# Performance work log

Measured on AMD Instinct MI355X. Metric: run time of the kernel, lower is better.

Reference implementation:

```python
import jax, jax.numpy as jnp
import numpy as np

N_USER, N_ITEM, D, K, E = 80000, 40000, 128, 10, 2000000

def _mlp(x, w1, b1, w2, b2, w3, b3):
    # MLP from source: linear->tanh->linear->tanh->linear->L2 normalize (eval mode, dropout off)
    x = jnp.tanh(x @ w1 + b1)
    x = jnp.tanh(x @ w2 + b2)
    x = x @ w3 + b3
    return x / jnp.maximum(jnp.linalg.norm(x, axis=-1, keepdims=True), 1e-12)

def setup_inputs() -> dict:
    key = jax.random.key(0)
    ks = jax.random.split(key, 24)
    s = 0.05
    inp = {
        'uemb_s': jax.random.normal(ks[0], (N_USER, D), jnp.float32),
        'iemb_s': jax.random.normal(ks[1], (N_ITEM, D), jnp.float32),
        'uemb_t': jax.random.normal(ks[2], (N_USER, D), jnp.float32),
        'u_emb_sp': jax.random.normal(ks[3], (N_USER, D), jnp.float32),
        'edge_user': jax.random.randint(ks[4], (E,), 0, N_USER, jnp.int32),
        'edge_item': jax.random.randint(ks[5], (E,), 0, N_ITEM, jnp.int32),
        # meta nets
        'Wu': jax.random.normal(ks[6], (4 * D, D), jnp.float32) * s,
        'bu': jnp.zeros((D,), jnp.float32),
        'Wi': jax.random.normal(ks[7], (2 * D, D), jnp.float32) * s,
        'bi': jnp.zeros((D,), jnp.float32),
        # mlp1: D -> D*K -> D//2 -> D*K
        'm1w1': jax.random.normal(ks[8], (D, D * K), jnp.float32) * s,
        'm1b1': jnp.zeros((D * K,), jnp.float32),
        'm1w2': jax.random.normal(ks[9], (D * K, D // 2), jnp.float32) * s,
        'm1b2': jnp.zeros((D // 2,), jnp.float32),
        'm1w3': jax.random.normal(ks[10], (D // 2, D * K), jnp.float32) * s,
        'm1b3': jnp.zeros((D * K,), jnp.float32),
        # mlp2: D -> D*K -> D//2 -> D*K
        'm2w1': jax.random.normal(ks[11], (D, D * K), jnp.float32) * s,
        'm2b1': jnp.zeros((D * K,), jnp.float32),
        'm2w2': jax.random.normal(ks[12], (D * K, D // 2), jnp.float32) * s,
        'm2b2': jnp.zeros((D // 2,), jnp.float32),
        'm2w3': jax.random.normal(ks[13], (D // 2, D * K), jnp.float32) * s,
        'm2b3': jnp.zeros((D * K,), jnp.float32),
    }
    return inp

def reference(uemb_s, iemb_s, uemb_t, u_emb_sp, edge_user, edge_item,
              Wu, bu, Wi, bi,
              m1w1, m1b1, m1w2, m1b2, m1w3, m1b3,
              m2w1, m2b1, m2w2, m2b2, m2w3, m2b3):
    # spmm with all-ones values == gather + segment_sum over the bipartite edge list
    neighbors_u = jax.ops.segment_sum(iemb_s[edge_item], edge_user, num_segments=N_USER)  # [U, D]
    tmp_embu = jax.lax.stop_gradient(
        jnp.concatenate([uemb_s, uemb_t, u_emb_sp, neighbors_u], axis=1)) @ Wu + bu       # [U, D]
    neighbors_i = jax.ops.segment_sum(((uemb_s + u_emb_sp) * 0.5)[edge_user], edge_item,
                                      num_segments=N_ITEM)                               # [I, D]
    tmp_embi = jax.lax.stop_gradient(
        jnp.concatenate([iemb_s, neighbors_i], axis=1)) @ Wi + bi                         # [I, D]
    metau = _mlp(tmp_embu, m1w1, m1b1, m1w2, m1b2, m1w3, m1b3).reshape(-1, D, K)          # [U, D, K]
    metai = _mlp(tmp_embi, m2w1, m2b1, m2w2, m2b2, m2w3, m2b3).reshape(-1, K, D)          # [I, K, D]
    meta_biasu = jnp.mean(metau, axis=0)  # [D, K]
    meta_biasi = jnp.mean(metai, axis=0)  # [K, D]
    low_weightu = jax.nn.softmax(metau + meta_biasu, axis=1)
    low_weighti = jax.nn.softmax(metai + meta_biasi, axis=1)
    return (low_weightu, low_weighti)
```

## Files before the change

### kernel.cpp

```cpp
#include <hip/hip_runtime.h>
#include <hip/hip_bf16.h>

#define D_ 128
#define DK_ 1280
#define K_ 10

typedef __attribute__((ext_vector_type(8))) short bh8;
typedef __attribute__((ext_vector_type(4))) short bh4;
typedef __attribute__((ext_vector_type(4))) float f32x4;

__device__ __forceinline__ short f2b(float f) {
    unsigned u = __builtin_bit_cast(unsigned, f);
    u += 0x7fffu + ((u >> 16) & 1u);
    return (short)(u >> 16);
}
__device__ __forceinline__ float b2f(short s) {
    unsigned u = ((unsigned)(unsigned short)s) << 16;
    return __builtin_bit_cast(float, u);
}
__device__ __forceinline__ float tanh_fast(float x) {
    float e = __expf(2.f * x);
    return 1.f - __fdividef(2.f, e + 1.f);
}
__device__ __forceinline__ f32x4 mfma16(bh8 a, bh8 b, f32x4 c) {
    return __builtin_amdgcn_mfma_f32_16x16x32_bf16(a, b, c, 0, 0, 0);
}

__device__ __forceinline__ int blk_excl_scan(int v, int t) {
    __shared__ int wp[4];
    int lane = t & 63, w = t >> 6;
    int s = v;
    for (int o = 1; o < 64; o <<= 1) {
        int pv = __shfl_up(s, o);
        if (lane >= o) s += pv;
    }
    if (lane == 63) wp[w] = s;
    __syncthreads();
    if (t == 0) {
        int a = 0;
#pragma unroll
        for (int k = 0; k < 4; ++k) { int x = wp[k]; wp[k] = a; a += x; }
    }
    __syncthreads();
    int r = s - v + wp[w];
    __syncthreads();
    return r;
}

__global__ __launch_bounds__(256) void cvt_all(
    const float* __restrict__ us, const float* __restrict__ ut,
    const float* __restrict__ usp, const float* __restrict__ is_,
    short* __restrict__ usb, short* __restrict__ utb,
    short* __restrict__ uspb, short* __restrict__ uavg, short* __restrict__ isb,
    int n4u, int n4i)
{
    int i = blockIdx.x * 256 + threadIdx.x;
    if (i < n4u) {
        float4 a = ((const float4*)us)[i];
        float4 b = ((const float4*)ut)[i];
        float4 c = ((const float4*)usp)[i];
        bh4 sa, sb, sc, sv;
        sa[0] = f2b(a.x); sa[1] = f2b(a.y); sa[2] = f2b(a.z); sa[3] = f2b(a.w);
        sb[0] = f2b(b.x); sb[1] = f2b(b.y); sb[2] = f2b(b.z); sb[3] = f2b(b.w);
        sc[0] = f2b(c.x); sc[1] = f2b(c.y); sc[2] = f2b(c.z); sc[3] = f2b(c.w);
        sv[0] = f2b(0.5f * (a.x + c.x)); sv[1] = f2b(0.5f * (a.y + c.y));
        sv[2] = f2b(0.5f * (a.z + c.z)); sv[3] = f2b(0.5f * (a.w + c.w));
        ((bh4*)usb)[i] = sa; ((bh4*)utb)[i] = sb;
        ((bh4*)uspb)[i] = sc; ((bh4*)uavg)[i] = sv;
    } else if (i < n4u + n4i) {
        int j = i - n4u;
        float4 v = ((const float4*)is_)[j];
        bh4 s;
        s[0] = f2b(v.x); s[1] = f2b(v.y); s[2] = f2b(v.z); s[3] = f2b(v.w);
        ((bh4*)isb)[j] = s;
    }
}

struct PackArgs {
    const float* W[8];
    short* o[8];
    int K[8];
    int N[8];
};
__global__ __launch_bounds__(256) void pack_all(PackArgs pa)
{
    int seg = blockIdx.y;
    int K = pa.K[seg], N = pa.N[seg];
    int total = K * N;
    int o = blockIdx.x * 256 + threadIdx.x;
    if (o >= total) return;
    const float* W = pa.W[seg];
    short* out = pa.o[seg];
    int j    = o & 7;
    int lane = (o >> 3) & 63;
    int rest = o >> 9;
    int KK = K >> 5;
    int kk = rest % KK;
    int tile = rest / KK;
    int k = kk * 32 + (lane >> 4) * 8 + j;
    int n = tile * 16 + (lane & 15);
    out[o] = f2b(W[(size_t)k * N + n]);
}

__global__ __launch_bounds__(256) void bhist_kernel(
    const int* __restrict__ eu, const int* __restrict__ ei,
    int* __restrict__ bcu, int* __restrict__ bci,
    int E, int shu, int shi, int nbu, int nbi)
{
    __shared__ int hu[160], hi[160];
    int t = threadIdx.x;
    int base = blockIdx.x * 4096;
    if (t < 160) { hu[t] = 0; hi[t] = 0; }
    __syncthreads();
    int n = min(4096, E - base);
#pragma unroll 4
    for (int k = 0; k < 16; ++k) {
        int idx = k * 256 + t;
        if (idx < n) {
            atomicAdd(&hu[eu[base + idx] >> shu], 1);
            atomicAdd(&hi[ei[base + idx] >> shi], 1);
        }
    }
    __syncthreads();
    if (t < nbu && hu[t]) atomicAdd(&bcu[t], hu[t]);
    if (t < nbi && hi[t]) atomicAdd(&bci[t], hi[t]);
}

__global__ __launch_bounds__(256) void binit_kernel(
    const int* __restrict__ bcu, int* __restrict__ gcu, int* __restrict__ bbu, int nbu,
    const int* __restrict__ bci, int* __restrict__ gci, int* __restrict__ bbi, int nbi,
    int E)
{
    int t = threadIdx.x;
    {
        int v = (t < nbu) ? bcu[t] : 0;
        int ex = blk_excl_scan(v, t);
        if (t < nbu) { gcu[t] = ex; bbu[t] = ex; }
        if (t == 0) bbu[nbu] = E;
    }
    __syncthreads();
    {
        int v = (t < nbi) ? bci[t] : 0;
        int ex = blk_excl_scan(v, t);
        if (t < nbi) { gci[t] = ex; bbi[t] = ex; }
        if (t == 0) bbi[nbi] = E;
    }
}

__global__ __launch_bounds__(256) void partition_kernel(
    const int* __restrict__ eu, const int* __restrict__ ei,
    int* __restrict__ gcu, int* __restrict__ gci,
    uint2* __restrict__ ebu, uint2* __restrict__ ebi,
    int E, int shu, int shi, int nbu, int nbi)
{
    __shared__ int hu[160], hi[160];
    int t = threadIdx.x;
    int base = blockIdx.x * 4096;
    if (t < 160) { hu[t] = 0; hi[t] = 0; }
    __syncthreads();
    int n = min(4096, E - base);
    int us[16], is_[16];
#pragma unroll 4
    for (int k = 0; k < 16; ++k) {
        int idx = k * 256 + t;
        if (idx < n) {
            us[k] = eu[base + idx];
            is_[k] = ei[base + idx];
            atomicAdd(&hu[us[k] >> shu], 1);
            atomicAdd(&hi[is_[k] >> shi], 1);
        } else us[k] = -1;
    }
    __syncthreads();
    if (t < nbu) { int c = hu[t]; hu[t] = c ? atomicAdd(&gcu[t], c) : 0; }
    if (t < nbi) { int c = hi[t]; hi[t] = c ? atomicAdd(&gci[t], c) : 0; }
    __syncthreads();
#pragma unroll 4
    for (int k = 0; k < 16; ++k) {
        if (us[k] >= 0) {
            int p1 = atomicAdd(&hu[us[k] >> shu], 1);
            ebu[p1] = make_uint2((unsigned)us[k], (unsigned)is_[k]);
            int p2 = atomicAdd(&hi[is_[k] >> shi], 1);
            ebi[p2] = make_uint2((unsigned)is_[k], (unsigned)us[k]);
        }
    }
}

__global__ __launch_bounds__(256) void fill2_all(
    const uint2* __restrict__ ebu, const int* __restrict__ bbu,
    int* __restrict__ off_u, int* __restrict__ end_u, int* __restrict__ adj_u,
    int NBU, int U,
    const uint2* __restrict__ ebi, const int* __restrict__ bbi,
    int* __restrict__ off_i, int* __restrict__ end_i, int* __restrict__ adj_i, int I)
{
    __shared__ int lcnt[512];
    __shared__ int lcur[512];
    bool isU = (int)blockIdx.x < NBU;
    const uint2* ebuf = isU ? ebu : ebi;
    const int* bbase  = isU ? bbu : bbi;
    int* off  = isU ? off_u : off_i;
    int* end_ = isU ? end_u : end_i;
    int* adj  = isU ? adj_u : adj_i;
    int span_sh = isU ? 9 : 8;
    int nrows = isU ? U : I;
    int b = isU ? blockIdx.x : blockIdx.x - NBU;

    int t = threadIdx.x;
    int rbase = b << span_sh;
    int span = min(1 << span_sh, nrows - rbase);
    int regbeg = bbase[b], regend = bbase[b + 1];
    for (int j = t; j < span; j += 256) lcnt[j] = 0;
    __syncthreads();
    for (int e = regbeg + t; e < regend; e += 256)
        atomicAdd(&lcnt[ebuf[e].x - rbase], 1);
    __syncthreads();
    int c0 = (2 * t < span) ? lcnt[2 * t] : 0;
    int c1 = (2 * t + 1 < span) ? lcnt[2 * t + 1] : 0;
    int ex = blk_excl_scan(c0 + c1, t);
    if (2 * t < span) {
        int beg = regbeg + ex;
        off[rbase + 2 * t] = beg;
        end_[rbase + 2 * t] = beg + c0;
        lcur[2 * t] = beg;
    }
    if (2 * t + 1 < span) {
        int beg = regbeg + ex + c0;
        off[rbase + 2 * t + 1] = beg;
        end_[rbase + 2 * t + 1] = beg + c1;
        lcur[2 * t + 1] = beg;
    }
    __syncthreads();
    for (int e = regbeg + t; e < regend; e += 256) {
        uint2 p = ebuf[e];
        int slot = atomicAdd(&lcur[p.x - rbase], 1);
        adj[slot] = (int)p.y;
    }
}

__global__ __launch_bounds__(256) void gather_all(
    const short* __restrict__ embU, const short* __restrict__ embI,
    const int* __restrict__ off_u, const int* __restrict__ end_u, const int* __restrict__ adj_u,
    const int* __restrict__ off_i, const int* __restrict__ end_i, const int* __restrict__ adj_i,
    short* __restrict__ nub, short* __restrict__ nib, int U, int I)
{
    int gw = (blockIdx.x * 256 + threadIdx.x) >> 6;
    int lane = threadIdx.x & 63;
    const short* emb; const int *offp, *endp, *adjp; short* outp; int row;
    if (gw < U)          { emb = embU; offp = off_u; endp = end_u; adjp = adj_u; outp = nub; row = gw; }
    else if (gw < U + I) { emb = embI; offp = off_i; endp = end_i; adjp = adj_i; outp = nib; row = gw - U; }
    else return;

    int beg = offp[row], end = endp[row];
    float ax = 0.f, ay = 0.f;
    int j = beg;
    for (; j + 3 < end; j += 4) {
        unsigned a = *(const unsigned*)(emb + (size_t)adjp[j]     * D_ + lane * 2);
        unsigned b = *(const unsigned*)(emb + (size_t)adjp[j + 1] * D_ + lane * 2);
        unsigned c = *(const unsigned*)(emb + (size_t)adjp[j + 2] * D_ + lane * 2);
        unsigned d = *(const unsigned*)(emb + (size_t)adjp[j + 3] * D_ + lane * 2);
        ax += b2f((short)(a & 0xffff)) + b2f((short)(b & 0xffff))
            + b2f((short)(c & 0xffff)) + b2f((short)(d & 0xffff));
        ay += b2f((short)(a >> 16)) + b2f((short)(b >> 16))
            + b2f((short)(c >> 16)) + b2f((short)(d >> 16));
    }
    for (; j < end; ++j) {
        unsigned a = *(const unsigned*)(emb + (size_t)adjp[j] * D_ + lane * 2);
        ax += b2f((short)(a & 0xffff));
        ay += b2f((short)(a >> 16));
    }
    unsigned o = ((unsigned)(unsigned short)f2b(ay) << 16) | (unsigned short)(unsigned)f2b(ax);
    *(unsigned*)(outp + (size_t)row * D_ + lane * 2) = o;
}

struct MlpArgs {
    const short *uA0, *uA1, *uA2, *uA3;
    const short *iA0, *iA1;
    const short *uWg, *uW1, *uW2, *uW3;
    const short *iWg, *iW1, *iW2, *iW3;
    const float *ubg, *ub1, *ub2, *ub3;
    const float *ibg, *ib1, *ib2, *ib3;
    short *uY, *iY;
    float *uNrm, *iNrm;
    int UB;
};

__global__ __launch_bounds__(256, 4) void fused_mlp_all(MlpArgs P)
{
    __shared__ char pool[35328];
    short* x2   = (short*)pool;
    short* h1q  = (short*)(pool + 8704);
    short* h2   = (short*)(pool + 29696);
    float* wred = (float*)(pool + 34304);

    const int t = threadIdx.x;
    const int l = t & 63;
    const int w = t >> 6;
    const int lr = l & 15;
    const int lg = l >> 4;

    const bool isU = (int)blockIdx.x < P.UB;
    const int bid = isU ? (int)blockIdx.x : (int)blockIdx.x - P.UB;
    const size_t rb0 = (size_t)bid * 32;
    const int KKG  = isU ? 16 : 8;
    const short* Wg = isU ? P.uWg : P.iWg;
    const short* W1 = isU ? P.uW1 : P.iW1;
    const short* W2 = isU ? P.uW2 : P.iW2;
    const short* W3 = isU ? P.uW3 : P.iW3;
    const float* bg = isU ? P.ubg : P.ibg;
    const float* b1 = isU ? P.ub1 : P.ib1;
    const float* b2 = isU ? P.ub2 : P.ib2;
    const float* b3 = isU ? P.ub3 : P.ib3;
    short* Ybf = isU ? P.uY : P.iY;
    float* Nrm = isU ? P.uNrm : P.iNrm;
    const short* srcs[4];
    if (isU) { srcs[0] = P.uA0; srcs[1] = P.uA1; srcs[2] = P.uA2; srcs[3] = P.uA3; }
    else     { srcs[0] = P.iA0; srcs[1] = P.iA1; srcs[2] = P.iA0; srcs[3] = P.iA1; }

    {
        f32x4 acc[2][2] = {{{0,0,0,0},{0,0,0,0}},{{0,0,0,0},{0,0,0,0}}};
        const short* wp = Wg + (size_t)(2 * w) * KKG * 512 + l * 8;
        const short* wq = wp + (size_t)KKG * 512;
        for (int kk = 0; kk < KKG; ++kk) {
            const short* src = srcs[kk >> 2];
            int coff = (kk & 3) * 32 + lg * 8;
            bh8 x0 = *(const bh8*)(src + (rb0 + lr) * D_ + coff);
            bh8 x1 = *(const bh8*)(src + (rb0 + 16 + lr) * D_ + coff);
            bh8 w0 = *(const bh8*)wp; wp += 512;
            bh8 w1 = *(const bh8*)wq; wq += 512;
            acc[0][0] = mfma16(w0, x0, acc[0][0]);
            acc[1][0] = mfma16(w0, x1, acc[1][0]);
            acc[0][1] = mfma16(w1, x0, acc[0][1]);
            acc[1][1] = mfma16(w1, x1, acc[1][1]);
        }
        float4 c0 = *(const float4*)(bg + (2 * w) * 16 + lg * 4);
        float4 c1 = *(const float4*)(bg + (2 * w + 1) * 16 + lg * 4);
#pragma unroll
        for (int rg = 0; rg < 2; ++rg) {
            bh4 p0, p1;
            p0[0] = f2b(acc[rg][0][0] + c0.x); p0[1] = f2b(acc[rg][0][1] + c0.y);
            p0[2] = f2b(acc[rg][0][2] + c0.z); p0[3] = f2b(acc[rg][0][3] + c0.w);
            p1[0] = f2b(acc[rg][1][0] + c1.x); p1[1] = f2b(acc[rg][1][1] + c1.y);
            p1[2] = f2b(acc[rg][1][2] + c1.z); p1[3] = f2b(acc[rg][1][3] + c1.w);
            *(bh4*)(x2 + (rg * 16 + lr) * 136 + (2 * w) * 16 + lg * 4) = p0;
            *(bh4*)(x2 + (rg * 16 + lr) * 136 + (2 * w + 1) * 16 + lg * 4) = p1;
        }
    }
    __syncthreads();

    bh8 xf[2][4];
#pragma unroll
    for (int rg = 0; rg < 2; ++rg)
#pragma unroll
        for (int kk = 0; kk < 4; ++kk)
            xf[rg][kk] = *(const bh8*)(x2 + (rg * 16 + lr) * 136 + kk * 32 + lg * 8);

    f32x4 c2[2][2] = {{{0,0,0,0},{0,0,0,0}},{{0,0,0,0},{0,0,0,0}}};
#pragma unroll 1
    for (int q = 0; q < 4; ++q) {
        const short* wp = W1 + (size_t)(q * 20 + w * 5) * 2048 + l * 8;
        const float* bp = b1 + (q * 20 + w * 5) * 16 + lg * 4;
#pragma unroll 1
        for (int tt = 0; tt < 5; ++tt) {
            f32x4 a0 = {0,0,0,0}, a1 = a0;
#pragma unroll
            for (int kk = 0; kk < 4; ++kk) {
                bh8 wf = *(const bh8*)wp; wp += 512;
                a0 = mfma16(wf, xf[0][kk], a0);
                a1 = mfma16(wf, xf[1][kk], a1);
            }
            float4 bv = *(const float4*)bp; bp += 16;
            bh4 pk0, pk1;
            pk0[0] = f2b(tanh_fast(a0[0] + bv.x)); pk0[1] = f2b(tanh_fast(a0[1] + bv.y));
            pk0[2] = f2b(tanh_fast(a0[2] + bv.z)); pk0[3] = f2b(tanh_fast(a0[3] + bv.w));
            pk1[0] = f2b(tanh_fast(a1[0] + bv.x)); pk1[1] = f2b(tanh_fast(a1[1] + bv.y));
            pk1[2] = f2b(tanh_fast(a1[2] + bv.z)); pk1[3] = f2b(tanh_fast(a1[3] + bv.w));
            int lt = w * 5 + tt;
            *(bh4*)(h1q + lr * 328 + lt * 16 + lg * 4) = pk0;
            *(bh4*)(h1q + (16 + lr) * 328 + lt * 16 + lg * 4) = pk1;
        }
        __syncthreads();
        const short* wp2 = W2 + (size_t)(w * 40 + q * 10) * 512 + l * 8;
        const short* hq0 = h1q + lr * 328 + lg * 8;
        const short* hq1 = h1q + (16 + lr) * 328 + lg * 8;
#pragma unroll 2
        for (int kk = 0; kk < 10; ++kk) {
            bh8 wf = *(const bh8*)wp2; wp2 += 512;
            bh8 h0 = *(const bh8*)(hq0 + kk * 32);
            bh8 h1v = *(const bh8*)(hq1 + kk * 32);
            if (kk & 1) { c2[0][1] = mfma16(wf, h0, c2[0][1]); c2[1][1] = mfma16(wf, h1v, c2[1][1]); }
            else        { c2[0][0] = mfma16(wf, h0, c2[0][0]); c2[1][0] = mfma16(wf, h1v, c2[1][0]); }
        }
        __syncthreads();
    }

    {
        float4 bv = *(const float4*)(b2 + w * 16 + lg * 4);
#pragma unroll
        for (int rg = 0; rg < 2; ++rg) {
            bh4 p2;
            p2[0] = f2b(tanh_fast(c2[rg][0][0] + c2[rg][1][0] + bv.x));
            p2[1] = f2b(tanh_fast(c2[rg][0][1] + c2[rg][1][1] + bv.y));
            p2[2] = f2b(tanh_fast(c2[rg][0][2] + c2[rg][1][2] + bv.z));
            p2[3] = f2b(tanh_fast(c2[rg][0][3] + c2[rg][1][3] + bv.w));
            *(bh4*)(h2 + (rg * 16 + lr) * 72 + w * 16 + lg * 4) = p2;
        }
    }
    __syncthreads();

    {
        bh8 hf[2][2];
#pragma unroll
        for (int rg = 0; rg < 2; ++rg) {
            hf[rg][0] = *(const bh8*)(h2 + (rg * 16 + lr) * 72 + lg * 8);
            hf[rg][1] = *(const bh8*)(h2 + (rg * 16 + lr) * 72 + 32 + lg * 8);
        }
        float ssq0 = 0.f, ssq1 = 0.f;
        const short* wp3 = W3 + (size_t)(w * 20) * 1024 + l * 8;
        const float* bp3 = b3 + w * 320 + lg * 4;
        short* dst0 = Ybf + (rb0 + lr) * DK_ + w * 320 + lg * 4;
        short* dst1 = Ybf + (rb0 + 16 + lr) * DK_ + w * 320 + lg * 4;
#pragma unroll 2
        for (int tt = 0; tt < 20; ++tt) {
            bh8 w0 = *(const bh8*)(wp3 + tt * 1024);
            bh8 w1 = *(const bh8*)(wp3 + tt * 1024 + 512);
            float4 bv = *(const float4*)(bp3 + tt * 16);
            f32x4 a0 = {0,0,0,0}, a1 = a0;
            a0 = mfma16(w0, hf[0][0], a0); a0 = mfma16(w1, hf[0][1], a0);
            a1 = mfma16(w0, hf[1][0], a1); a1 = mfma16(w1, hf[1][1], a1);
            float v00 = a0[0] + bv.x, v01 = a0[1] + bv.y, v02 = a0[2] + bv.z, v03 = a0[3] + bv.w;
            float v10 = a1[0] + bv.x, v11 = a1[1] + bv.y, v12 = a1[2] + bv.z, v13 = a1[3] + bv.w;
            ssq0 = fmaf(v00, v00, ssq0); ssq0 = fmaf(v01, v01, ssq0);
            ssq0 = fmaf(v02, v02, ssq0); ssq0 = fmaf(v03, v03, ssq0);
            ssq1 = fmaf(v10, v10, ssq1); ssq1 = fmaf(v11, v11, ssq1);
            ssq1 = fmaf(v12, v12, ssq1); ssq1 = fmaf(v13, v13, ssq1);
            bh4 o0, o1;
            o0[0] = f2b(v00); o0[1] = f2b(v01); o0[2] = f2b(v02); o0[3] = f2b(v03);
            o1[0] = f2b(v10); o1[1] = f2b(v11); o1[2] = f2b(v12); o1[3] = f2b(v13);
            *(bh4*)(dst0 + tt * 16) = o0;
            *(bh4*)(dst1 + tt * 16) = o1;
        }
        ssq0 += __shfl_xor(ssq0, 16); ssq0 += __shfl_xor(ssq0, 32);
        ssq1 += __shfl_xor(ssq1, 16); ssq1 += __shfl_xor(ssq1, 32);
        if (l < 16) {
            wred[w * 32 + l] = ssq0;
            wred[w * 32 + 16 + l] = ssq1;
        }
    }
    __syncthreads();
    if (t < 32) {
        float s = wred[t] + wred[32 + t] + wred[64 + t] + wred[96 + t];
        Nrm[rb0 + t] = 1.f / fmaxf(sqrtf(s), 1e-12f);
    }
}

__global__ __launch_bounds__(256) void finalize_bias(
    const short* __restrict__ Yu, const short* __restrict__ Yi,
    const float* __restrict__ nrmU, const float* __restrict__ nrmI,
    float* __restrict__ bsu, float* __restrict__ bsi, int U, int I, int NCH)
{
    int z = blockIdx.y;
    const short* Y = z ? Yi : Yu;
    const float* nr = z ? nrmI : nrmU;
    float* dst = z ? bsi : bsu;
    int M = z ? I : U;
    int chunk = (M + NCH - 1) / NCH;
    int r0 = blockIdx.x * chunk;
    int r1 = min(M, r0 + chunk);
    if (r0 >= r1) return;
    int t = threadIdx.x;
    float s0 = 0.f, s1 = 0.f, s2 = 0.f, s3 = 0.f, s4 = 0.f;
    for (int r = r0; r < r1; ++r) {
        const short* row = Y + (size_t)r * DK_;
        float nv = nr[r];
        s0 += b2f(row[t]) * nv;
        s1 += b2f(row[256 + t]) * nv;
        s2 += b2f(row[512 + t]) * nv;
        s3 += b2f(row[768 + t]) * nv;
        s4 += b2f(row[1024 + t]) * nv;
    }
    atomicAdd(&dst[t], s0);
    atomicAdd(&dst[256 + t], s1);
    atomicAdd(&dst[512 + t], s2);
    atomicAdd(&dst[768 + t], s3);
    atomicAdd(&dst[1024 + t], s4);
}

__global__ __launch_bounds__(64) void softmax_all(
    const short* __restrict__ Yu, const short* __restrict__ Yi,
    const float* __restrict__ nrmU, const float* __restrict__ nrmI,
    const float* __restrict__ bsu, const float* __restrict__ bsi,
    float invU, float invI,
    float* __restrict__ outu, float* __restrict__ outi, int U, int I)
{
    __shared__ float rowb[DK_];
    int b = blockIdx.x;
    int t = threadIdx.x;
    if (b < U) {
        size_t base = (size_t)b * DK_;
        float nrm = nrmU[b];
        for (int i = t; i < DK_ / 4; i += 64) {
            uint2 a = ((const uint2*)(Yu + base))[i];
            float4 bv = ((const float4*)bsu)[i];
            rowb[4 * i + 0] = b2f((short)(a.x & 0xffff)) * nrm + bv.x * invU;
            rowb[4 * i + 1] = b2f((short)(a.x >> 16))    * nrm + bv.y * invU;
            rowb[4 * i + 2] = b2f((short)(a.y & 0xffff)) * nrm + bv.z * invU;
            rowb[4 * i + 3] = b2f((short)(a.y >> 16))    * nrm + bv.w * invU;
        }
        __syncthreads();
#pragma unroll 1
        for (int k = 0; k < K_; ++k) {
            float v0 = rowb[t * K_ + k];
            float v1 = rowb[(t + 64) * K_ + k];
            float m = fmaxf(v0, v1);
            for (int off = 32; off; off >>= 1) m = fmaxf(m, __shfl_xor(m, off));
            float e0 = expf(v0 - m), e1 = expf(v1 - m);
            float s = e0 + e1;
            for (int off = 32; off; off >>= 1) s += __shfl_xor(s, off);
            float rs = 1.f / s;
            rowb[t * K_ + k] = e0 * rs;
            rowb[(t + 64) * K_ + k] = e1 * rs;
        }
        __syncthreads();
        for (int i = t; i < DK_ / 4; i += 64)
            ((float4*)(outu + base))[i] = ((const float4*)rowb)[i];
    } else {
        int it = b - U;
        if (it >= I) return;
        size_t base = (size_t)it * DK_;
        float nrm = nrmI[it];
        float v0[K_], v1[K_];
        float m0 = -1e30f, m1 = -1e30f;
#pragma unroll
        for (int k = 0; k < K_; ++k) {
            unsigned a = *(const unsigned*)(Yi + base + k * D_ + 2 * t);
            float2 bv = ((const float2*)(bsi + k * D_))[t];
            v0[k] = b2f((short)(a & 0xffff)) * nrm + bv.x * invI;
            v1[k] = b2f((short)(a >> 16))    * nrm + bv.y * invI;
            m0 = fmaxf(m0, v0[k]); m1 = fmaxf(m1, v1[k]);
        }
        float s0 = 0.f, s1 = 0.f;
#pragma unroll
        for (int k = 0; k < K_; ++k) {
            v0[k] = expf(v0[k] - m0); s0 += v0[k];
            v1[k] = expf(v1[k] - m1); s1 += v1[k];
        }
        float r0 = 1.f / s0, r1 = 1.f / s1;
#pragma unroll
        for (int k = 0; k < K_; ++k) {
            float2 o; o.x = v0[k] * r0; o.y = v1[k] * r1;
            ((float2*)(outi + base + k * D_))[t] = o;
        }
    }
}

extern "C" void kernel_launch(void* const* d_in, const int* in_sizes, int n_in,
                              void* d_out, int out_size, void* d_ws, size_t ws_size,
                              hipStream_t stream)
{
    const float* uemb_s   = (const float*)d_in[0];
    const float* iemb_s   = (const float*)d_in[1];
    const float* uemb_t   = (const float*)d_in[2];
    const float* u_emb_sp = (const float*)d_in[3];
    const int*   eu       = (const int*)d_in[4];
    const int*   ei       = (const int*)d_in[5];
    const float* Wu  = (const float*)d_in[6];
    const float* bu  = (const float*)d_in[7];
    const float* Wi  = (const float*)d_in[8];
    const float* bi  = (const float*)d_in[9];
    const float* m1w1 = (const float*)d_in[10];
    const float* m1b1 = (const float*)d_in[11];
    const float* m1w2 = (const float*)d_in[12];
    const float* m1b2 = (const float*)d_in[13];
    const float* m1w3 = (const float*)d_in[14];
    const float* m1b3 = (const float*)d_in[15];
    const float* m2w1 = (const float*)d_in[16];
    const float* m2b1 = (const float*)d_in[17];
    const float* m2w2 = (const float*)d_in[18];
    const float* m2b2 = (const float*)d_in[19];
    const float* m2w3 = (const float*)d_in[20];
    const float* m2b3 = (const float*)d_in[21];

    const int U = in_sizes[0] / D_;
    const int I = in_sizes[1] / D_;
    const int E = in_sizes[4];

    const int SHU = 9, SHI = 8;
    const int NBU = (U + 511) >> 9;
    const int NBI = (I + 255) >> 8;
    const int UB = U / 32, IB = I / 32;

    char* p = (char*)d_ws;
    auto alloc = [&](size_t bytes) { char* r = p; p += (bytes + 255) & ~(size_t)255; return r; };

    short* usb  = (short*)alloc((size_t)U * D_ * 2);
    short* utb  = (short*)alloc((size_t)U * D_ * 2);
    short* uspb = (short*)alloc((size_t)U * D_ * 2);
    short* uavg = (short*)alloc((size_t)U * D_ * 2);
    short* isb  = (short*)alloc((size_t)I * D_ * 2);
    short* nub  = (short*)alloc((size_t)U * D_ * 2);
    short* nib  = (short*)alloc((size_t)I * D_ * 2);
    short* ybu  = (short*)alloc((size_t)U * DK_ * 2);
    short* ybi  = (short*)alloc((size_t)I * DK_ * 2);
    float* nrmU = (float*)alloc((size_t)U * 4);
    float* nrmI = (float*)alloc((size_t)I * 4);
    short* WgU  = (short*)alloc(512 * 128 * 2);
    short* WgI  = (short*)alloc(256 * 128 * 2);
    short* W1U  = (short*)alloc(128 * 1280 * 2);
    short* W2U  = (short*)alloc(1280 * 64 * 2);
    short* W3U  = (short*)alloc(64 * 1280 * 2);
    short* W1I  = (short*)alloc(128 * 1280 * 2);
    short* W2I  = (short*)alloc(1280 * 64 * 2);
    short* W3I  = (short*)alloc(64 * 1280 * 2);
    int*   zbuf = (int*)alloc((320 + 2 * DK_) * 4);
    int* bcnt_u = zbuf;
    int* bcnt_i = zbuf + 160;
    float* bsu  = (float*)(zbuf + 320);
    float* bsi  = bsu + DK_;
    int* gcur_u = (int*)alloc(160 * 4);
    int* gcur_i = (int*)alloc(160 * 4);
    int* bbase_u = (int*)alloc(161 * 4);
    int* bbase_i = (int*)alloc(161 * 4);
    int* off_u  = (int*)alloc((size_t)U * 4);
    int* end_u  = (int*)alloc((size_t)U * 4);
    int* off_i  = (int*)alloc((size_t)I * 4);
    int* end_i  = (int*)alloc((size_t)I * 4);
    uint2* ebu  = (uint2*)alloc((size_t)E * 8);
    uint2* ebi  = (uint2*)alloc((size_t)E * 8);
    int* adj_u  = (int*)alloc((size_t)E * 4);
    int* adj_i  = (int*)alloc((size_t)E * 4);

    float* outu = (float*)d_out;
    float* outi = outu + (size_t)U * DK_;

    hipMemsetAsync(zbuf, 0, (320 + 2 * DK_) * 4, stream);

    int n4u = U * D_ / 4, n4i = I * D_ / 4;
    cvt_all<<<(n4u + n4i + 255) / 256, 256, 0, stream>>>(
        uemb_s, uemb_t, u_emb_sp, iemb_s, usb, utb, uspb, uavg, isb, n4u, n4i);

    PackArgs pa;
    pa.W[0] = Wu;   pa.o[0] = WgU; pa.K[0] = 512;  pa.N[0] = 128;
    pa.W[1] = Wi;   pa.o[1] = WgI; pa.K[1] = 256;  pa.N[1] = 128;
    pa.W[2] = m1w1; pa.o[2] = W1U; pa.K[2] = 128;  pa.N[2] = 1280;
    pa.W[3] = m1w2; pa.o[3] = W2U; pa.K[3] = 1280; pa.N[3] = 64;
    pa.W[4] = m1w3; pa.o[4] = W3U; pa.K[4] = 64;   pa.N[4] = 1280;
    pa.W[5] = m2w1; pa.o[5] = W1I; pa.K[5] = 128;  pa.N[5] = 1280;
    pa.W[6] = m2w2; pa.o[6] = W2I; pa.K[6] = 1280; pa.N[6] = 64;
    pa.W[7] = m2w3; pa.o[7] = W3I; pa.K[7] = 64;   pa.N[7] = 1280;
    pack_all<<<dim3(640, 8), 256, 0, stream>>>(pa);

    int pb = (E + 4095) / 4096;
    bhist_kernel<<<pb, 256, 0, stream>>>(eu, ei, bcnt_u, bcnt_i, E, SHU, SHI, NBU, NBI);
    binit_kernel<<<1, 256, 0, stream>>>(bcnt_u, gcur_u, bbase_u, NBU,
                                        bcnt_i, gcur_i, bbase_i, NBI, E);
    partition_kernel<<<pb, 256, 0, stream>>>(eu, ei, gcur_u, gcur_i, ebu, ebi,
                                             E, SHU, SHI, NBU, NBI);
    fill2_all<<<NBU + NBI, 256, 0, stream>>>(ebu, bbase_u, off_u, end_u, adj_u, NBU, U,
                                             ebi, bbase_i, off_i, end_i, adj_i, I);

    gather_all<<<(U + I + 3) / 4, 256, 0, stream>>>(
        isb, uavg, off_u, end_u, adj_u, off_i, end_i, adj_i, nub, nib, U, I);

    MlpArgs ma;
    ma.uA0 = usb; ma.uA1 = utb; ma.uA2 = uspb; ma.uA3 = nub;
    ma.iA0 = isb; ma.iA1 = nib;
    ma.uWg = WgU; ma.uW1 = W1U; ma.uW2 = W2U; ma.uW3 = W3U;
    ma.iWg = WgI; ma.iW1 = W1I; ma.iW2 = W2I; ma.iW3 = W3I;
    ma.ubg = bu; ma.ub1 = m1b1; ma.ub2 = m1b2; ma.ub3 = m1b3;
    ma.ibg = bi; ma.ib1 = m2b1; ma.ib2 = m2b2; ma.ib3 = m2b3;
    ma.uY = ybu; ma.iY = ybi;
    ma.uNrm = nrmU; ma.iNrm = nrmI;
    ma.UB = UB;
    fused_mlp_all<<<UB + IB, 256, 0, stream>>>(ma);

    finalize_bias<<<dim3(256, 2), 256, 0, stream>>>(ybu, ybi, nrmU, nrmI, bsu, bsi, U, I, 256);

    softmax_all<<<U + I, 64, 0, stream>>>(ybu, ybi, nrmU, nrmI, bsu, bsi,
                                          1.0f / (float)U, 1.0f / (float)I, outu, outi, U, I);
}
```

Baseline: 929.4 us.

## Use 64-row MLP tiles, fuse column-mean partials, and pack edge buffers into 32 bits

The fused MLP now processes 64 rows per block instead of 32, so each weight fragment load feeds four row groups of MFMAs. The h1 chunking is restructured to 10 slices of 128 columns, reusing LDS space. The block also computes per-column normalized partial sums for the mean bias and writes them out, so finalize_bias only reduces a small partial buffer instead of re-reading the whole Y matrix. Separately, the partition buffers pack the local row offset and neighbor index into one 32-bit word, halving the edge-bucket traffic. Risks are higher register pressure with fewer blocks launched, and an extra re-read of freshly written Y from cache inside the MLP kernel.

```diff
diff --git a/kernel.cpp b/kernel.cpp
--- a/kernel.cpp
+++ b/kernel.cpp
@@ -150,7 +150,7 @@
 __global__ __launch_bounds__(256) void partition_kernel(
     const int* __restrict__ eu, const int* __restrict__ ei,
     int* __restrict__ gcu, int* __restrict__ gci,
-    uint2* __restrict__ ebu, uint2* __restrict__ ebi,
+    unsigned* __restrict__ ebu, unsigned* __restrict__ ebi,
     int E, int shu, int shi, int nbu, int nbi)
 {
     __shared__ int hu[160], hi[160];
@@ -178,29 +178,31 @@
     for (int k = 0; k < 16; ++k) {
         if (us[k] >= 0) {
             int p1 = atomicAdd(&hu[us[k] >> shu], 1);
-            ebu[p1] = make_uint2((unsigned)us[k], (unsigned)is_[k]);
+            ebu[p1] = ((unsigned)(us[k] & 511) << 16) | (unsigned)is_[k];
             int p2 = atomicAdd(&hi[is_[k] >> shi], 1);
-            ebi[p2] = make_uint2((unsigned)is_[k], (unsigned)us[k]);
+            ebi[p2] = ((unsigned)(is_[k] & 255) << 17) | (unsigned)us[k];
         }
     }
 }
 
 __global__ __launch_bounds__(256) void fill2_all(
-    const uint2* __restrict__ ebu, const int* __restrict__ bbu,
+    const unsigned* __restrict__ ebu, const int* __restrict__ bbu,
     int* __restrict__ off_u, int* __restrict__ end_u, int* __restrict__ adj_u,
     int NBU, int U,
-    const uint2* __restrict__ ebi, const int* __restrict__ bbi,
+    const unsigned* __restrict__ ebi, const int* __restrict__ bbi,
     int* __restrict__ off_i, int* __restrict__ end_i, int* __restrict__ adj_i, int I)
 {
     __shared__ int lcnt[512];
     __shared__ int lcur[512];
     bool isU = (int)blockIdx.x < NBU;
-    const uint2* ebuf = isU ? ebu : ebi;
+    const unsigned* ebuf = isU ? ebu : ebi;
     const int* bbase  = isU ? bbu : bbi;
     int* off  = isU ? off_u : off_i;
     int* end_ = isU ? end_u : end_i;
     int* adj  = isU ? adj_u : adj_i;
     int span_sh = isU ? 9 : 8;
+    int pay_sh = isU ? 16 : 17;
+    unsigned pmask = (1u << pay_sh) - 1u;
     int nrows = isU ? U : I;
     int b = isU ? blockIdx.x : blockIdx.x - NBU;
 
@@ -211,7 +213,7 @@
     for (int j = t; j < span; j += 256) lcnt[j] = 0;
     __syncthreads();
     for (int e = regbeg + t; e < regend; e += 256)
-        atomicAdd(&lcnt[ebuf[e].x - rbase], 1);
+        atomicAdd(&lcnt[ebuf[e] >> pay_sh], 1);
     __syncthreads();
     int c0 = (2 * t < span) ? lcnt[2 * t] : 0;
     int c1 = (2 * t + 1 < span) ? lcnt[2 * t + 1] : 0;
@@ -230,9 +232,9 @@
     }
     __syncthreads();
     for (int e = regbeg + t; e < regend; e += 256) {
-        uint2 p = ebuf[e];
-        int slot = atomicAdd(&lcur[p.x - rbase], 1);
-        adj[slot] = (int)p.y;
+        unsigned p = ebuf[e];
+        int slot = atomicAdd(&lcur[p >> pay_sh], 1);
+        adj[slot] = (int)(p & pmask);
     }
 }
 
@@ -280,16 +282,19 @@
     const float *ibg, *ib1, *ib2, *ib3;
     short *uY, *iY;
     float *uNrm, *iNrm;
+    float *partial;
     int UB;
 };
 
 __global__ __launch_bounds__(256, 4) void fused_mlp_all(MlpArgs P)
 {
-    __shared__ char pool[35328];
+    __shared__ char pool[33024];
     short* x2   = (short*)pool;
-    short* h1q  = (short*)(pool + 8704);
-    short* h2   = (short*)(pool + 29696);
-    float* wred = (float*)(pool + 34304);
+    short* h1q  = (short*)pool;
+    short* h2   = (short*)(pool + 17408);
+    float* wred = (float*)(pool + 26624);
+    float* nrmS = (float*)(pool + 27648);
+    float* part = (float*)(pool + 27904);
 
     const int t = threadIdx.x;
     const int l = t & 63;
@@ -299,7 +304,7 @@
 
     const bool isU = (int)blockIdx.x < P.UB;
     const int bid = isU ? (int)blockIdx.x : (int)blockIdx.x - P.UB;
-    const size_t rb0 = (size_t)bid * 32;
+    const size_t rb0 = (size_t)bid * 64;
     const int KKG  = isU ? 16 : 8;
     const short* Wg = isU ? P.uWg : P.iWg;
     const short* W1 = isU ? P.uW1 : P.iW1;
@@ -316,25 +321,26 @@
     else     { srcs[0] = P.iA0; srcs[1] = P.iA1; srcs[2] = P.iA0; srcs[3] = P.iA1; }
 
     {
-        f32x4 acc[2][2] = {{{0,0,0,0},{0,0,0,0}},{{0,0,0,0},{0,0,0,0}}};
+        f32x4 acc[4][2] = {{{0,0,0,0},{0,0,0,0}},{{0,0,0,0},{0,0,0,0}},
+                           {{0,0,0,0},{0,0,0,0}},{{0,0,0,0},{0,0,0,0}}};
         const short* wp = Wg + (size_t)(2 * w) * KKG * 512 + l * 8;
         const short* wq = wp + (size_t)KKG * 512;
         for (int kk = 0; kk < KKG; ++kk) {
             const short* src = srcs[kk >> 2];
             int coff = (kk & 3) * 32 + lg * 8;
-            bh8 x0 = *(const bh8*)(src + (rb0 + lr) * D_ + coff);
-            bh8 x1 = *(const bh8*)(src + (rb0 + 16 + lr) * D_ + coff);
             bh8 w0 = *(const bh8*)wp; wp += 512;
             bh8 w1 = *(const bh8*)wq; wq += 512;
-            acc[0][0] = mfma16(w0, x0, acc[0][0]);
-            acc[1][0] = mfma16(w0, x1, acc[1][0]);
-            acc[0][1] = mfma16(w1, x0, acc[0][1]);
-            acc[1][1] = mfma16(w1, x1, acc[1][1]);
+#pragma unroll
+            for (int rg = 0; rg < 4; ++rg) {
+                bh8 xv = *(const bh8*)(src + (rb0 + rg * 16 + lr) * D_ + coff);
+                acc[rg][0] = mfma16(w0, xv, acc[rg][0]);
+                acc[rg][1] = mfma16(w1, xv, acc[rg][1]);
+            }
         }
         float4 c0 = *(const float4*)(bg + (2 * w) * 16 + lg * 4);
         float4 c1 = *(const float4*)(bg + (2 * w + 1) * 16 + lg * 4);
 #pragma unroll
-        for (int rg = 0; rg < 2; ++rg) {
+        for (int rg = 0; rg < 4; ++rg) {
             bh4 p0, p1;
             p0[0] = f2b(acc[rg][0][0] + c0.x); p0[1] = f2b(acc[rg][0][1] + c0.y);
             p0[2] = f2b(acc[rg][0][2] + c0.z); p0[3] = f2b(acc[rg][0][3] + c0.w);
@@ -346,48 +352,51 @@
     }
     __syncthreads();
 
-    bh8 xf[2][4];
-#pragma unroll
-    for (int rg = 0; rg < 2; ++rg)
+    bh8 xf[4][4];
+#pragma unroll
+    for (int rg = 0; rg < 4; ++rg)
 #pragma unroll
         for (int kk = 0; kk < 4; ++kk)
             xf[rg][kk] = *(const bh8*)(x2 + (rg * 16 + lr) * 136 + kk * 32 + lg * 8);
-
-    f32x4 c2[2][2] = {{{0,0,0,0},{0,0,0,0}},{{0,0,0,0},{0,0,0,0}}};
+    __syncthreads();
+
+    f32x4 c2[4] = {{0,0,0,0},{0,0,0,0},{0,0,0,0},{0,0,0,0}};
 #pragma unroll 1
-    for (int q = 0; q < 4; ++q) {
-        const short* wp = W1 + (size_t)(q * 20 + w * 5) * 2048 + l * 8;
-        const float* bp = b1 + (q * 20 + w * 5) * 16 + lg * 4;
+    for (int q = 0; q < 10; ++q) {
 #pragma unroll 1
-        for (int tt = 0; tt < 5; ++tt) {
-            f32x4 a0 = {0,0,0,0}, a1 = a0;
+        for (int tt = 0; tt < 2; ++tt) {
+            int gt = q * 8 + w * 2 + tt;
+            const short* wp = W1 + (size_t)gt * 2048 + l * 8;
+            f32x4 a[4] = {{0,0,0,0},{0,0,0,0},{0,0,0,0},{0,0,0,0}};
 #pragma unroll
             for (int kk = 0; kk < 4; ++kk) {
                 bh8 wf = *(const bh8*)wp; wp += 512;
-                a0 = mfma16(wf, xf[0][kk], a0);
-                a1 = mfma16(wf, xf[1][kk], a1);
+#pragma unroll
+                for (int rg = 0; rg < 4; ++rg)
+                    a[rg] = mfma16(wf, xf[rg][kk], a[rg]);
             }
-            float4 bv = *(const float4*)bp; bp += 16;
-            bh4 pk0, pk1;
-            pk0[0] = f2b(tanh_fast(a0[0] + bv.x)); pk0[1] = f2b(tanh_fast(a0[1] + bv.y));
-            pk0[2] = f2b(tanh_fast(a0[2] + bv.z)); pk0[3] = f2b(tanh_fast(a0[3] + bv.w));
-            pk1[0] = f2b(tanh_fast(a1[0] + bv.x)); pk1[1] = f2b(tanh_fast(a1[1] + bv.y));
-            pk1[2] = f2b(tanh_fast(a1[2] + bv.z)); pk1[3] = f2b(tanh_fast(a1[3] + bv.w));
-            int lt = w * 5 + tt;
-            *(bh4*)(h1q + lr * 328 + lt * 16 + lg * 4) = pk0;
-            *(bh4*)(h1q + (16 + lr) * 328 + lt * 16 + lg * 4) = pk1;
+            float4 bv = *(const float4*)(b1 + gt * 16 + lg * 4);
+            int lt = (w * 2 + tt) * 16;
+#pragma unroll
+            for (int rg = 0; rg < 4; ++rg) {
+                bh4 pk;
+                pk[0] = f2b(tanh_fast(a[rg][0] + bv.x));
+                pk[1] = f2b(tanh_fast(a[rg][1] + bv.y));
+                pk[2] = f2b(tanh_fast(a[rg][2] + bv.z));
+                pk[3] = f2b(tanh_fast(a[rg][3] + bv.w));
+                *(bh4*)(h1q + (rg * 16 + lr) * 136 + lt + lg * 4) = pk;
+            }
         }
         __syncthreads();
-        const short* wp2 = W2 + (size_t)(w * 40 + q * 10) * 512 + l * 8;
-        const short* hq0 = h1q + lr * 328 + lg * 8;
-        const short* hq1 = h1q + (16 + lr) * 328 + lg * 8;
-#pragma unroll 2
-        for (int kk = 0; kk < 10; ++kk) {
+        const short* wp2 = W2 + ((size_t)w * 40 + q * 4) * 512 + l * 8;
+#pragma unroll
+        for (int kk = 0; kk < 4; ++kk) {
             bh8 wf = *(const bh8*)wp2; wp2 += 512;
-            bh8 h0 = *(const bh8*)(hq0 + kk * 32);
-            bh8 h1v = *(const bh8*)(hq1 + kk * 32);
-            if (kk & 1) { c2[0][1] = mfma16(wf, h0, c2[0][1]); c2[1][1] = mfma16(wf, h1v, c2[1][1]); }
-            else        { c2[0][0] = mfma16(wf, h0, c2[0][0]); c2[1][0] = mfma16(wf, h1v, c2[1][0]); }
+#pragma unroll
+            for (int rg = 0; rg < 4; ++rg) {
+                bh8 hf = *(const bh8*)(h1q + (rg * 16 + lr) * 136 + kk * 32 + lg * 8);
+                c2[rg] = mfma16(wf, hf, c2[rg]);
+            }
         }
         __syncthreads();
     }
@@ -395,93 +404,111 @@
     {
         float4 bv = *(const float4*)(b2 + w * 16 + lg * 4);
 #pragma unroll
-        for (int rg = 0; rg < 2; ++rg) {
+        for (int rg = 0; rg < 4; ++rg) {
             bh4 p2;
-            p2[0] = f2b(tanh_fast(c2[rg][0][0] + c2[rg][1][0] + bv.x));
-            p2[1] = f2b(tanh_fast(c2[rg][0][1] + c2[rg][1][1] + bv.y));
-            p2[2] = f2b(tanh_fast(c2[rg][0][2] + c2[rg][1][2] + bv.z));
-            p2[3] = f2b(tanh_fast(c2[rg][0][3] + c2[rg][1][3] + bv.w));
+            p2[0] = f2b(tanh_fast(c2[rg][0] + bv.x));
+            p2[1] = f2b(tanh_fast(c2[rg][1] + bv.y));
+            p2[2] = f2b(tanh_fast(c2[rg][2] + bv.z));
+            p2[3] = f2b(tanh_fast(c2[rg][3] + bv.w));
             *(bh4*)(h2 + (rg * 16 + lr) * 72 + w * 16 + lg * 4) = p2;
         }
     }
     __syncthreads();
 
     {
-        bh8 hf[2][2];
-#pragma unroll
-        for (int rg = 0; rg < 2; ++rg) {
+        bh8 hf[4][2];
+#pragma unroll
+        for (int rg = 0; rg < 4; ++rg) {
             hf[rg][0] = *(const bh8*)(h2 + (rg * 16 + lr) * 72 + lg * 8);
             hf[rg][1] = *(const bh8*)(h2 + (rg * 16 + lr) * 72 + 32 + lg * 8);
         }
-        float ssq0 = 0.f, ssq1 = 0.f;
+        float ssq[4] = {0.f, 0.f, 0.f, 0.f};
         const short* wp3 = W3 + (size_t)(w * 20) * 1024 + l * 8;
         const float* bp3 = b3 + w * 320 + lg * 4;
-        short* dst0 = Ybf + (rb0 + lr) * DK_ + w * 320 + lg * 4;
-        short* dst1 = Ybf + (rb0 + 16 + lr) * DK_ + w * 320 + lg * 4;
 #pragma unroll 2
         for (int tt = 0; tt < 20; ++tt) {
             bh8 w0 = *(const bh8*)(wp3 + tt * 1024);
             bh8 w1 = *(const bh8*)(wp3 + tt * 1024 + 512);
             float4 bv = *(const float4*)(bp3 + tt * 16);
-            f32x4 a0 = {0,0,0,0}, a1 = a0;
-            a0 = mfma16(w0, hf[0][0], a0); a0 = mfma16(w1, hf[0][1], a0);
-            a1 = mfma16(w0, hf[1][0], a1); a1 = mfma16(w1, hf[1][1], a1);
-            float v00 = a0[0] + bv.x, v01 = a0[1] + bv.y, v02 = a0[2] + bv.z, v03 = a0[3] + bv.w;
-            float v10 = a1[0] + bv.x, v11 = a1[1] + bv.y, v12 = a1[2] + bv.z, v13 = a1[3] + bv.w;
-            ssq0 = fmaf(v00, v00, ssq0); ssq0 = fmaf(v01, v01, ssq0);
-            ssq0 = fmaf(v02, v02, ssq0); ssq0 = fmaf(v03, v03, ssq0);
-            ssq1 = fmaf(v10, v10, ssq1); ssq1 = fmaf(v11, v11, ssq1);
-            ssq1 = fmaf(v12, v12, ssq1); ssq1 = fmaf(v13, v13, ssq1);
-            bh4 o0, o1;
-            o0[0] = f2b(v00); o0[1] = f2b(v01); o0[2] = f2b(v02); o0[3] = f2b(v03);
-            o1[0] = f2b(v10); o1[1] = f2b(v11); o1[2] = f2b(v12); o1[3] = f2b(v13);
-            *(bh4*)(dst0 + tt * 16) = o0;
-            *(bh4*)(dst1 + tt * 16) = o1;
-        }
-        ssq0 += __shfl_xor(ssq0, 16); ssq0 += __shfl_xor(ssq0, 32);
-        ssq1 += __shfl_xor(ssq1, 16); ssq1 += __shfl_xor(ssq1, 32);
-        if (l < 16) {
-            wred[w * 32 + l] = ssq0;
-            wred[w * 32 + 16 + l] = ssq1;
-        }
-    }
-    __syncthreads();
-    if (t < 32) {
-        float s = wred[t] + wred[32 + t] + wred[64 + t] + wred[96 + t];
-        Nrm[rb0 + t] = 1.f / fmaxf(sqrtf(s), 1e-12f);
-    }
+#pragma unroll
+            for (int rg = 0; rg < 4; ++rg) {
+                f32x4 a = {0, 0, 0, 0};
+                a = mfma16(w0, hf[rg][0], a);
+                a = mfma16(w1, hf[rg][1], a);
+                float v0 = a[0] + bv.x, v1 = a[1] + bv.y;
+                float v2 = a[2] + bv.z, v3 = a[3] + bv.w;
+                ssq[rg] = fmaf(v0, v0, ssq[rg]); ssq[rg] = fmaf(v1, v1, ssq[rg]);
+                ssq[rg] = fmaf(v2, v2, ssq[rg]); ssq[rg] = fmaf(v3, v3, ssq[rg]);
+                bh4 o;
+                o[0] = f2b(v0); o[1] = f2b(v1); o[2] = f2b(v2); o[3] = f2b(v3);
+                *(bh4*)(Ybf + (rb0 + rg * 16 + lr) * DK_ + w * 320 + lg * 4 + tt * 16) = o;
+            }
+        }
+#pragma unroll
+        for (int rg = 0; rg < 4; ++rg) {
+            float s = ssq[rg];
+            s += __shfl_xor(s, 16);
+            s += __shfl_xor(s, 32);
+            if (l < 16) wred[w * 64 + rg * 16 + l] = s;
+        }
+    }
+    __syncthreads();
+    if (t < 64) {
+        float s = wred[t] + wred[64 + t] + wred[128 + t] + wred[192 + t];
+        float nv = 1.f / fmaxf(sqrtf(s), 1e-12f);
+        nrmS[t] = nv;
+        Nrm[rb0 + t] = nv;
+    }
+    __syncthreads();
+
+    {
+        float nv[4];
+#pragma unroll
+        for (int rg = 0; rg < 4; ++rg) nv[rg] = nrmS[rg * 16 + lr];
+        const short* dstb = Ybf + (rb0 + lr) * DK_ + w * 320 + lg * 4;
+#pragma unroll 2
+        for (int tt = 0; tt < 20; ++tt) {
+            float s0 = 0.f, s1 = 0.f, s2 = 0.f, s3 = 0.f;
+#pragma unroll
+            for (int rg = 0; rg < 4; ++rg) {
+                bh4 v = *(const bh4*)(dstb + (size_t)rg * 16 * DK_ + tt * 16);
+                s0 = fmaf(b2f(v[0]), nv[rg], s0);
+                s1 = fmaf(b2f(v[1]), nv[rg], s1);
+                s2 = fmaf(b2f(v[2]), nv[rg], s2);
+                s3 = fmaf(b2f(v[3]), nv[rg], s3);
+            }
+#pragma unroll
+            for (int o = 1; o < 16; o <<= 1) {
+                s0 += __shfl_xor(s0, o); s1 += __shfl_xor(s1, o);
+                s2 += __shfl_xor(s2, o); s3 += __shfl_xor(s3, o);
+            }
+            if (lr == 0) {
+                float* pp = part + w * 320 + tt * 16 + lg * 4;
+                pp[0] = s0; pp[1] = s1; pp[2] = s2; pp[3] = s3;
+            }
+        }
+    }
+    __syncthreads();
+    for (int c = t; c < DK_; c += 256)
+        P.partial[(size_t)blockIdx.x * DK_ + c] = part[c];
 }
 
 __global__ __launch_bounds__(256) void finalize_bias(
-    const short* __restrict__ Yu, const short* __restrict__ Yi,
-    const float* __restrict__ nrmU, const float* __restrict__ nrmI,
-    float* __restrict__ bsu, float* __restrict__ bsi, int U, int I, int NCH)
-{
-    int z = blockIdx.y;
-    const short* Y = z ? Yi : Yu;
-    const float* nr = z ? nrmI : nrmU;
+    const float* __restrict__ partial,
+    float* __restrict__ bsu, float* __restrict__ bsi, int UB, int IB, int NCH)
+{
+    int c = blockIdx.x * 256 + threadIdx.x;
+    int z = blockIdx.z;
+    const float* base = partial + (z ? (size_t)UB * DK_ : 0);
     float* dst = z ? bsi : bsu;
-    int M = z ? I : U;
+    int M = z ? IB : UB;
     int chunk = (M + NCH - 1) / NCH;
-    int r0 = blockIdx.x * chunk;
+    int r0 = blockIdx.y * chunk;
     int r1 = min(M, r0 + chunk);
     if (r0 >= r1) return;
-    int t = threadIdx.x;
-    float s0 = 0.f, s1 = 0.f, s2 = 0.f, s3 = 0.f, s4 = 0.f;
-    for (int r = r0; r < r1; ++r) {
-        const short* row = Y + (size_t)r * DK_;
-        float nv = nr[r];
-        s0 += b2f(row[t]) * nv;
-        s1 += b2f(row[256 + t]) * nv;
-        s2 += b2f(row[512 + t]) * nv;
-        s3 += b2f(row[768 + t]) * nv;
-        s4 += b2f(row[1024 + t]) * nv;
-    }
-    atomicAdd(&dst[t], s0);
-    atomicAdd(&dst[256 + t], s1);
-    atomicAdd(&dst[512 + t], s2);
-    atomicAdd(&dst[768 + t], s3);
-    atomicAdd(&dst[1024 + t], s4);
+    float s = 0.f;
+    for (int r = r0; r < r1; ++r) s += base[(size_t)r * DK_ + c];
+    atomicAdd(&dst[c], s);
 }
 
 __global__ __launch_bounds__(64) void softmax_all(
@@ -586,7 +613,7 @@
     const int SHU = 9, SHI = 8;
     const int NBU = (U + 511) >> 9;
     const int NBI = (I + 255) >> 8;
-    const int UB = U / 32, IB = I / 32;
+    const int UB = U / 64, IB = I / 64;
 
     char* p = (char*)d_ws;
     auto alloc = [&](size_t bytes) { char* r = p; p += (bytes + 255) & ~(size_t)255; return r; };
@@ -602,6 +629,7 @@
     short* ybi  = (short*)alloc((size_t)I * DK_ * 2);
     float* nrmU = (float*)alloc((size_t)U * 4);
     float* nrmI = (float*)alloc((size_t)I * 4);
+    float* partial = (float*)alloc((size_t)(UB + IB) * DK_ * 4);
     short* WgU  = (short*)alloc(512 * 128 * 2);
     short* WgI  = (short*)alloc(256 * 128 * 2);
     short* W1U  = (short*)alloc(128 * 1280 * 2);
@@ -623,8 +651,8 @@
     int* end_u  = (int*)alloc((size_t)U * 4);
     int* off_i  = (int*)alloc((size_t)I * 4);
     int* end_i  = (int*)alloc((size_t)I * 4);
-    uint2* ebu  = (uint2*)alloc((size_t)E * 8);
-    uint2* ebi  = (uint2*)alloc((size_t)E * 8);
+    unsigned* ebu = (unsigned*)alloc((size_t)E * 4);
+    unsigned* ebi = (unsigned*)alloc((size_t)E * 4);
     int* adj_u  = (int*)alloc((size_t)E * 4);
     int* adj_i  = (int*)alloc((size_t)E * 4);
 
@@ -669,10 +697,11 @@
     ma.ibg = bi; ma.ib1 = m2b1; ma.ib2 = m2b2; ma.ib3 = m2b3;
     ma.uY = ybu; ma.iY = ybi;
     ma.uNrm = nrmU; ma.iNrm = nrmI;
+    ma.partial = partial;
     ma.UB = UB;
     fused_mlp_all<<<UB + IB, 256, 0, stream>>>(ma);
 
-    finalize_bias<<<dim3(256, 2), 256, 0, stream>>>(ybu, ybi, nrmU, nrmI, bsu, bsi, U, I, 256);
+    finalize_bias<<<dim3(5, 8, 2), 256, 0, stream>>>(partial, bsu, bsi, UB, IB, 8);
 
     softmax_all<<<U + I, 64, 0, stream>>>(ybu, ybi, nrmU, nrmI, bsu, bsi,
                                           1.0f / (float)U, 1.0f / (float)I, outu, outi, U, I);
```

Result: faster. 905.4 us (-2.6%).
